# Kernel optimization log

Measured on AMD Instinct MI355X. Metric: run time of the kernel, lower is better.

Reference implementation:

```python
import jax, jax.numpy as jnp
import numpy as np
from jax import lax

K = 5          # kernel_size
P = K // 2     # padding
DN = ('NCHW', 'OIHW', 'NCHW')


def _dwconv(z, wt, bt):
    # depthwise conv: z [b,c,h,w], wt [c,1,K,K], bt [c]
    c = z.shape[1]
    y = lax.conv_general_dilated(z, wt, (1, 1), [(P, P), (P, P)],
                                 feature_group_count=c, dimension_numbers=DN)
    return y + bt[None, :, None, None]


def setup_inputs() -> dict:
    key = jax.random.key(0)
    ks = jax.random.split(key, 8)
    b, c, h, w = 8, 64, 256, 256
    return {
        'x': jax.random.normal(ks[0], (b, c, h, w), jnp.float32),
        'w1': jax.random.normal(ks[1], (3, c, 1, K, K), jnp.float32) * 0.1,
        'b1': jax.random.normal(ks[2], (3, c), jnp.float32) * 0.1,
        'w2': jax.random.normal(ks[3], (3, c, 1, K, K), jnp.float32) * 0.1,
        'b2': jax.random.normal(ks[4], (3, c), jnp.float32) * 0.1,
        'wk': jax.random.normal(ks[5], (K * K * c, c), jnp.float32) * 0.1,
        'bk': jax.random.normal(ks[6], (K * K * c,), jnp.float32) * 0.1,
        'bias': jnp.zeros((c,), jnp.float32),
    }


def reference(x, w1, b1, w2, b2, wk, bk, bias):
    b, c, h, w = x.shape
    # avgpool 2x2 stride 2
    t = x.reshape(b, c, h // 2, 2, w // 2, 2).mean(axis=(3, 5))
    # Block1: 3 depthwise convs
    for i in range(3):
        t = _dwconv(t, w1[i], b1[i])
    # maxpool 2x2 stride 2
    hh, ww = t.shape[2], t.shape[3]
    t = t.reshape(b, c, hh // 2, 2, ww // 2, 2).max(axis=(3, 5))
    # Block2: 3 depthwise convs
    for i in range(3):
        t = _dwconv(t, w2[i], b2[i])
    # adaptive avg pool to 1x1 -> [b, c]
    g = t.mean(axis=(2, 3))
    # tokernel 1x1 conv -> per-sample depthwise kernels [b*c, 1, K, K]
    kern = (jnp.einsum('bc,oc->bo', g, wk) + bk).reshape(b * c, 1, K, K)
    # per-sample dynamic depthwise conv (groups = b*c)
    y = lax.conv_general_dilated(x.reshape(1, b * c, h, w), kern, (1, 1),
                                 [(P, P), (P, P)], feature_group_count=b * c,
                                 dimension_numbers=DN)
    return y.reshape(b, c, h, w) + bias[None, :, None, None]
```

## Files before the change

kernel.cpp:

```cpp
#include <hip/hip_runtime.h>

#define CC 64
#define HH 256
#define WW 256
#define SROW 140
#define BROW 76

template<int SS>
__device__ __forceinline__ void conv4x4_e12(const float* __restrict__ rb,
                                            const float* __restrict__ w,
                                            float bv, float a[4][4])
{
#pragma unroll
    for (int i = 0; i < 4; i++)
#pragma unroll
        for (int j = 0; j < 4; j++) a[i][j] = bv;
#pragma unroll
    for (int ir = 0; ir < 8; ir++) {
        const float* s = rb + ir * SS;
        float4 A = *(const float4*)s;
        float4 B = *(const float4*)(s + 4);
        float4 C = *(const float4*)(s + 8);
        float e[12] = {A.x, A.y, A.z, A.w, B.x, B.y, B.z, B.w,
                       C.x, C.y, C.z, C.w};
#pragma unroll
        for (int i = 0; i < 4; i++) {
            const int ky = ir - i;
            if (ky >= 0 && ky < 5) {
#pragma unroll
                for (int kx = 0; kx < 5; kx++) {
                    const float wv = w[ky * 5 + kx];
#pragma unroll
                    for (int j = 0; j < 4; j++) a[i][j] += e[j + kx + 2] * wv;
                }
            }
        }
    }
}

__device__ __forceinline__ void conv1x4_e12B(const float* __restrict__ rb,
                                             const float* __restrict__ w,
                                             float bv, float a[4])
{
#pragma unroll
    for (int j = 0; j < 4; j++) a[j] = bv;
#pragma unroll
    for (int ir = 0; ir < 5; ir++) {
        const float* s = rb + ir * BROW;
        float4 A = *(const float4*)s;
        float4 B = *(const float4*)(s + 4);
        float4 C = *(const float4*)(s + 8);
        float e[12] = {A.x, A.y, A.z, A.w, B.x, B.y, B.z, B.w,
                       C.x, C.y, C.z, C.w};
#pragma unroll
        for (int kx = 0; kx < 5; kx++) {
            const float wv = w[ir * 5 + kx];
#pragma unroll
            for (int j = 0; j < 4; j++) a[j] += e[j + kx + 2] * wv;
        }
    }
}

__global__ __launch_bounds__(512, 4) void k_keff(
    const float* __restrict__ w2, const float* __restrict__ b2,
    float* __restrict__ kq, float* __restrict__ beta)
{
    const int c = blockIdx.x;
    const int tid = threadIdx.x;
    __shared__ __align__(16) float sb[68 * BROW];
    __shared__ float red[16];

    for (int i = tid; i < 68 * 19; i += 512) {
        int r = i / 19, q = i % 19;
        int d = 4 * q;
        float4 v = make_float4(0.f, 0.f, 0.f, 0.f);
        if (r >= 2 && r < 66 && d >= 8 && d < 72)
            v = make_float4(1.f, 1.f, 1.f, 1.f);
        *(float4*)&sb[r * BROW + d] = v;
    }
    __syncthreads();

    const int r0 = tid >> 4;
    const int u = tid & 15;
    float S0 = 0.f, S1 = 0.f;

#pragma unroll
    for (int step = 0; step < 2; step++) {
        const int cv = 2 - step;
        float w[25];
#pragma unroll
        for (int k = 0; k < 25; k++) w[k] = w2[cv * CC * 25 + c * 25 + (24 - k)];
        float a0[4], a1[4];
        conv1x4_e12B(&sb[r0 * BROW + 4 * u + 4], w, 0.f, a0);
        conv1x4_e12B(&sb[(r0 + 32) * BROW + 4 * u + 4], w, 0.f, a1);
        __syncthreads();
        *(float4*)&sb[(r0 + 2) * BROW + 8 + 4 * u] = make_float4(a0[0], a0[1], a0[2], a0[3]);
        *(float4*)&sb[(r0 + 34) * BROW + 8 + 4 * u] = make_float4(a1[0], a1[1], a1[2], a1[3]);
        float s = a0[0] + a0[1] + a0[2] + a0[3] + a1[0] + a1[1] + a1[2] + a1[3];
        if (step == 0) S0 += s; else S1 += s;
        __syncthreads();
    }

    {
        float w[25];
#pragma unroll
        for (int k = 0; k < 25; k++) w[k] = w2[0 * CC * 25 + c * 25 + (24 - k)];
        float a0[4], a1[4];
        conv1x4_e12B(&sb[r0 * BROW + 4 * u + 4], w, 0.f, a0);
        conv1x4_e12B(&sb[(r0 + 32) * BROW + 4 * u + 4], w, 0.f, a1);
        __syncthreads();
        *(float4*)&sb[(r0 + 2) * BROW + 8 + 4 * u] = make_float4(a0[0], a0[1], a0[2], a0[3]);
        *(float4*)&sb[(r0 + 34) * BROW + 8 + 4 * u] = make_float4(a1[0], a1[1], a1[2], a1[3]);
        __syncthreads();
    }

    for (int i = tid; i < 1024; i += 512) {
        int v = i >> 5, uu = i & 31;
        float k00 = sb[(2 * v + 2) * BROW + 8 + 2 * uu];
        float k01 = sb[(2 * v + 2) * BROW + 8 + 2 * uu + 1];
        float k10 = sb[(2 * v + 3) * BROW + 8 + 2 * uu];
        float k11 = sb[(2 * v + 3) * BROW + 8 + 2 * uu + 1];
        *(float4*)&kq[((size_t)(c * 32 + v) * 32 + uu) * 4] =
            make_float4(k00 * (1.f / 4096.f), k01 * (1.f / 4096.f),
                        k10 * (1.f / 4096.f), k11 * (1.f / 4096.f));
    }

#pragma unroll
    for (int off = 32; off > 0; off >>= 1) {
        S0 += __shfl_down(S0, off);
        S1 += __shfl_down(S1, off);
    }
    if ((tid & 63) == 0) { red[tid >> 6] = S0; red[8 + (tid >> 6)] = S1; }
    __syncthreads();
    if (tid == 0) {
        float t0 = 0.f, t1 = 0.f;
#pragma unroll
        for (int k = 0; k < 8; k++) { t0 += red[k]; t1 += red[8 + k]; }
        beta[c] = (b2[0 * CC + c] * t1 + b2[1 * CC + c] * t0 +
                   4096.f * b2[2 * CC + c]) * (1.f / 4096.f);
    }
}

__global__ __launch_bounds__(1024, 8) void k_a(
    const float* __restrict__ x, const float* __restrict__ w1,
    const float* __restrict__ b1, const float* __restrict__ kq,
    const float* __restrict__ beta, float* __restrict__ g)
{
    const int plane = blockIdx.x;
    const int c = plane & 63;
    const int tid = threadIdx.x;

    __shared__ __align__(16) float sb[132 * SROW];
    __shared__ float red[16];

    const float* xp = x + (size_t)plane * HH * WW;

#pragma unroll
    for (int k = 0; k < 5; k++) {
        int i = tid + k * 1024;
        if (i < 132 * 35) {
            int r = i / 35, f = i % 35;
            int d = 4 * f;
            float4 v = make_float4(0.f, 0.f, 0.f, 0.f);
            int p = r - 2;
            if (d >= 8 && d < 136 && (unsigned)p < 128u) {
                int xc = 2 * (d - 8);
                const float* p0 = xp + (size_t)(2 * p) * WW + xc;
                const float* p1 = p0 + WW;
                float4 a0 = *(const float4*)p0;
                float4 a1 = *(const float4*)(p0 + 4);
                float4 b0 = *(const float4*)p1;
                float4 b1v = *(const float4*)(p1 + 4);
                v.x = 0.25f * (a0.x + a0.y + b0.x + b0.y);
                v.y = 0.25f * (a0.z + a0.w + b0.z + b0.w);
                v.z = 0.25f * (a1.x + a1.y + b1v.x + b1v.y);
                v.w = 0.25f * (a1.z + a1.w + b1v.z + b1v.w);
            }
            *(float4*)&sb[r * SROW + d] = v;
        }
    }
    __syncthreads();

    const int v = tid >> 5, u = tid & 31;
    const float* rbA = &sb[(4 * v) * SROW + 4 * u + 4];
    float* wbA = &sb[(4 * v + 2) * SROW + 8 + 4 * u];

#pragma unroll
    for (int cv = 0; cv < 2; cv++) {
        float w[25];
#pragma unroll
        for (int k = 0; k < 25; k++) w[k] = w1[cv * CC * 25 + c * 25 + k];
        const float bv = b1[cv * CC + c];
        float a[4][4];
        conv4x4_e12<SROW>(rbA, w, bv, a);
        __syncthreads();
#pragma unroll
        for (int i = 0; i < 4; i++)
            *(float4*)(wbA + i * SROW) = make_float4(a[i][0], a[i][1], a[i][2], a[i][3]);
        __syncthreads();
    }

    float partial;
    {
        float w[25];
#pragma unroll
        for (int k = 0; k < 25; k++) w[k] = w1[2 * CC * 25 + c * 25 + k];
        const float bv = b1[2 * CC + c];
        float a[4][4];
        conv4x4_e12<SROW>(rbA, w, bv, a);
        float m00 = fmaxf(fmaxf(a[0][0], a[0][1]), fmaxf(a[1][0], a[1][1]));
        float m01 = fmaxf(fmaxf(a[0][2], a[0][3]), fmaxf(a[1][2], a[1][3]));
        float m10 = fmaxf(fmaxf(a[2][0], a[2][1]), fmaxf(a[3][0], a[3][1]));
        float m11 = fmaxf(fmaxf(a[2][2], a[2][3]), fmaxf(a[3][2], a[3][3]));
        float4 kk = *(const float4*)&kq[((size_t)(c * 32 + v) * 32 + u) * 4];
        partial = m00 * kk.x + m01 * kk.y + m10 * kk.z + m11 * kk.w;
    }
#pragma unroll
    for (int off = 32; off > 0; off >>= 1) partial += __shfl_down(partial, off);
    if ((tid & 63) == 0) red[tid >> 6] = partial;
    __syncthreads();
    if (tid == 0) {
        float t = 0.f;
#pragma unroll
        for (int k = 0; k < 16; k++) t += red[k];
        g[plane] = t + beta[c];
    }
}

__global__ __launch_bounds__(256) void k_kern(
    const float* __restrict__ g, const float* __restrict__ wk,
    const float* __restrict__ bk, float* __restrict__ kern)
{
    const int o = blockIdx.x * 256 + threadIdx.x;
    const int b = o / 1600, oo = o - b * 1600;
    float v = bk[oo];
    const float* wp = wk + (size_t)oo * 64;
    const float* gp = g + b * 64;
#pragma unroll 16
    for (int k = 0; k < 64; k++) v += gp[k] * wp[k];
    kern[o] = v;
}

__global__ __launch_bounds__(256) void k_dyn(
    const float* __restrict__ x, const float* __restrict__ kern,
    const float* __restrict__ bias, float* __restrict__ out)
{
    const int plane = blockIdx.z;
    const int tx = blockIdx.x, ty = blockIdx.y;
    const int tid = threadIdx.x;

    __shared__ __align__(16) float sx[68 * 76];

    const float* xp = x + (size_t)plane * HH * WW;
    const int R0 = ty * 64, C0 = tx * 64;

#pragma unroll
    for (int k = 0; k < 5; k++) {
        int i = tid + k * 256;
        if (i < 68 * 18) {
            int r = i / 18, q = i - r * 18;
            int gr = R0 - 2 + r;
            int gc = C0 - 4 + 4 * q;
            float4 v = make_float4(0.f, 0.f, 0.f, 0.f);
            if ((unsigned)gr < HH && (unsigned)gc < WW)
                v = *(const float4*)(xp + (size_t)gr * WW + gc);
            *(float4*)&sx[r * 76 + 4 * q] = v;
        }
    }

    float w[25];
#pragma unroll
    for (int k = 0; k < 25; k++) w[k] = kern[(size_t)plane * 25 + k];
    const float bv = bias[plane & 63];

    __syncthreads();

    const int tr = (tid >> 4) * 4, tc = (tid & 15) * 4;
    float acc[4][4];
    conv4x4_e12<76>(&sx[tr * 76 + tc], w, bv, acc);

    float* op = out + (size_t)plane * HH * WW + (size_t)(R0 + tr) * WW + C0 + tc;
#pragma unroll
    for (int i = 0; i < 4; i++)
        *(float4*)(op + (size_t)i * WW) = make_float4(acc[i][0], acc[i][1], acc[i][2], acc[i][3]);
}

extern "C" void kernel_launch(void* const* d_in, const int* in_sizes, int n_in,
                              void* d_out, int out_size, void* d_ws, size_t ws_size,
                              hipStream_t stream)
{
    const float* x    = (const float*)d_in[0];
    const float* w1   = (const float*)d_in[1];
    const float* b1   = (const float*)d_in[2];
    const float* w2   = (const float*)d_in[3];
    const float* b2   = (const float*)d_in[4];
    const float* wk   = (const float*)d_in[5];
    const float* bk   = (const float*)d_in[6];
    const float* bias = (const float*)d_in[7];
    float* out = (float*)d_out;

    float* ws   = (float*)d_ws;
    float* kq   = ws;
    float* beta = ws + 262144;
    float* g    = ws + 262208;
    float* kern = ws + 262720;

    k_keff<<<dim3(64), 512, 0, stream>>>(w2, b2, kq, beta);
    k_a<<<dim3(512), 1024, 0, stream>>>(x, w1, b1, kq, beta, g);
    k_kern<<<dim3(50), 256, 0, stream>>>(g, wk, bk, kern);
    k_dyn<<<dim3(4, 4, 512), 256, 0, stream>>>(x, kern, bias, out);
}
```

Measured before the change: 114.6 us.

## Split k_a into half-plane row tiles with halo recompute and 4x8 register tiles

The pooled-branch kernel now processes each plane as two 64-row halves with a 6-row halo, using 512 threads and a smaller shared buffer. The halo rows are recomputed across the three chained convolutions, with the active thread count shrinking at each stage. Each thread now computes a 4x8 output tile instead of 4x4, which improves reuse of the loaded row segments. Partial sums per half are reduced in k_kern, which now runs one block per batch and caches g in shared memory. The intent is better occupancy and latency hiding, at the cost of redundant halo compute and idle threads in the later stages.

```diff
diff --git a/kernel.cpp b/kernel.cpp
--- a/kernel.cpp
+++ b/kernel.cpp
@@ -5,6 +5,29 @@
 #define WW 256
 #define SROW 140
 #define BROW 76
+
+__device__ __forceinline__ void conv1x4_e12B(const float* __restrict__ rb,
+                                             const float* __restrict__ w,
+                                             float bv, float a[4])
+{
+#pragma unroll
+    for (int j = 0; j < 4; j++) a[j] = bv;
+#pragma unroll
+    for (int ir = 0; ir < 5; ir++) {
+        const float* s = rb + ir * BROW;
+        float4 A = *(const float4*)s;
+        float4 B = *(const float4*)(s + 4);
+        float4 C = *(const float4*)(s + 8);
+        float e[12] = {A.x, A.y, A.z, A.w, B.x, B.y, B.z, B.w,
+                       C.x, C.y, C.z, C.w};
+#pragma unroll
+        for (int kx = 0; kx < 5; kx++) {
+            const float wv = w[ir * 5 + kx];
+#pragma unroll
+            for (int j = 0; j < 4; j++) a[j] += e[j + kx + 2] * wv;
+        }
+    }
+}
 
 template<int SS>
 __device__ __forceinline__ void conv4x4_e12(const float* __restrict__ rb,
@@ -38,25 +61,34 @@
     }
 }
 
-__device__ __forceinline__ void conv1x4_e12B(const float* __restrict__ rb,
-                                             const float* __restrict__ w,
-                                             float bv, float a[4])
-{
-#pragma unroll
-    for (int j = 0; j < 4; j++) a[j] = bv;
-#pragma unroll
-    for (int ir = 0; ir < 5; ir++) {
-        const float* s = rb + ir * BROW;
-        float4 A = *(const float4*)s;
-        float4 B = *(const float4*)(s + 4);
-        float4 C = *(const float4*)(s + 8);
-        float e[12] = {A.x, A.y, A.z, A.w, B.x, B.y, B.z, B.w,
-                       C.x, C.y, C.z, C.w};
-#pragma unroll
-        for (int kx = 0; kx < 5; kx++) {
-            const float wv = w[ir * 5 + kx];
-#pragma unroll
-            for (int j = 0; j < 4; j++) a[j] += e[j + kx + 2] * wv;
+__device__ __forceinline__ void conv4x8_e16(const float* __restrict__ rb,
+                                            const float* __restrict__ w,
+                                            float bv, float a[4][8])
+{
+#pragma unroll
+    for (int i = 0; i < 4; i++)
+#pragma unroll
+        for (int j = 0; j < 8; j++) a[i][j] = bv;
+#pragma unroll
+    for (int ir = 0; ir < 8; ir++) {
+        const float* s = rb + ir * SROW;
+        float e[16];
+#pragma unroll
+        for (int m = 0; m < 4; m++) {
+            float4 t = *(const float4*)(s + 4 * m);
+            e[4 * m] = t.x; e[4 * m + 1] = t.y; e[4 * m + 2] = t.z; e[4 * m + 3] = t.w;
+        }
+#pragma unroll
+        for (int i = 0; i < 4; i++) {
+            const int ky = ir - i;
+            if (ky >= 0 && ky < 5) {
+#pragma unroll
+                for (int kx = 0; kx < 5; kx++) {
+                    const float wv = w[ky * 5 + kx];
+#pragma unroll
+                    for (int j = 0; j < 8; j++) a[i][j] += e[j + kx + 2] * wv;
+                }
+            }
         }
     }
 }
@@ -100,7 +132,6 @@
         if (step == 0) S0 += s; else S1 += s;
         __syncthreads();
     }
-
     {
         float w[25];
 #pragma unroll
@@ -141,31 +172,33 @@
     }
 }
 
-__global__ __launch_bounds__(1024, 8) void k_a(
+__global__ __launch_bounds__(512, 6) void k_a(
     const float* __restrict__ x, const float* __restrict__ w1,
     const float* __restrict__ b1, const float* __restrict__ kq,
-    const float* __restrict__ beta, float* __restrict__ g)
-{
-    const int plane = blockIdx.x;
+    float* __restrict__ part)
+{
+    const int by = blockIdx.x;
+    const int plane = blockIdx.y;
     const int c = plane & 63;
+    const int R0 = by * 64;
     const int tid = threadIdx.x;
 
-    __shared__ __align__(16) float sb[132 * SROW];
-    __shared__ float red[16];
+    __shared__ __align__(16) float sb[76 * SROW];
+    __shared__ float red[8];
 
     const float* xp = x + (size_t)plane * HH * WW;
 
 #pragma unroll
-    for (int k = 0; k < 5; k++) {
-        int i = tid + k * 1024;
-        if (i < 132 * 35) {
+    for (int k = 0; k < 6; k++) {
+        int i = tid + k * 512;
+        if (i < 76 * 35) {
             int r = i / 35, f = i % 35;
             int d = 4 * f;
             float4 v = make_float4(0.f, 0.f, 0.f, 0.f);
-            int p = r - 2;
-            if (d >= 8 && d < 136 && (unsigned)p < 128u) {
+            int pr = R0 - 6 + r;
+            if (d >= 8 && d < 136 && (unsigned)pr < 128u) {
                 int xc = 2 * (d - 8);
-                const float* p0 = xp + (size_t)(2 * p) * WW + xc;
+                const float* p0 = xp + (size_t)(2 * pr) * WW + xc;
                 const float* p1 = p0 + WW;
                 float4 a0 = *(const float4*)p0;
                 float4 a1 = *(const float4*)(p0 + 4);
@@ -181,39 +214,89 @@
     }
     __syncthreads();
 
-    const int v = tid >> 5, u = tid & 31;
-    const float* rbA = &sb[(4 * v) * SROW + 4 * u + 4];
-    float* wbA = &sb[(4 * v + 2) * SROW + 8 + 4 * u];
-
-#pragma unroll
-    for (int cv = 0; cv < 2; cv++) {
-        float w[25];
-#pragma unroll
-        for (int k = 0; k < 25; k++) w[k] = w1[cv * CC * 25 + c * 25 + k];
-        const float bv = b1[cv * CC + c];
-        float a[4][4];
-        conv4x4_e12<SROW>(rbA, w, bv, a);
-        __syncthreads();
-#pragma unroll
-        for (int i = 0; i < 4; i++)
-            *(float4*)(wbA + i * SROW) = make_float4(a[i][0], a[i][1], a[i][2], a[i][3]);
-        __syncthreads();
-    }
-
-    float partial;
+    const int v = tid >> 4, u = tid & 15;
+
     {
         float w[25];
 #pragma unroll
+        for (int k = 0; k < 25; k++) w[k] = w1[0 * CC * 25 + c * 25 + k];
+        const float bv = b1[0 * CC + c];
+        const bool act = tid < 288;
+        float a[4][8];
+        if (act) {
+            conv4x8_e16(&sb[(4 * v) * SROW + 4 + 8 * u], w, bv, a);
+#pragma unroll
+            for (int i = 0; i < 4; i++) {
+                int gi = R0 - 4 + 4 * v + i;
+                if ((unsigned)gi >= 128u) {
+#pragma unroll
+                    for (int j = 0; j < 8; j++) a[i][j] = 0.f;
+                }
+            }
+        }
+        __syncthreads();
+        if (act) {
+#pragma unroll
+            for (int i = 0; i < 4; i++) {
+                float* row = &sb[(2 + 4 * v + i) * SROW + 8 + 8 * u];
+                *(float4*)row = make_float4(a[i][0], a[i][1], a[i][2], a[i][3]);
+                *(float4*)(row + 4) = make_float4(a[i][4], a[i][5], a[i][6], a[i][7]);
+            }
+        }
+        __syncthreads();
+    }
+
+    {
+        float w[25];
+#pragma unroll
+        for (int k = 0; k < 25; k++) w[k] = w1[1 * CC * 25 + c * 25 + k];
+        const float bv = b1[1 * CC + c];
+        const bool act = tid < 272;
+        float a[4][8];
+        if (act) {
+            conv4x8_e16(&sb[(2 + 4 * v) * SROW + 4 + 8 * u], w, bv, a);
+#pragma unroll
+            for (int i = 0; i < 4; i++) {
+                int gi = R0 - 2 + 4 * v + i;
+                if ((unsigned)gi >= 128u) {
+#pragma unroll
+                    for (int j = 0; j < 8; j++) a[i][j] = 0.f;
+                }
+            }
+        }
+        __syncthreads();
+        if (act) {
+#pragma unroll
+            for (int i = 0; i < 4; i++) {
+                float* row = &sb[(4 + 4 * v + i) * SROW + 8 + 8 * u];
+                *(float4*)row = make_float4(a[i][0], a[i][1], a[i][2], a[i][3]);
+                *(float4*)(row + 4) = make_float4(a[i][4], a[i][5], a[i][6], a[i][7]);
+            }
+        }
+        __syncthreads();
+    }
+
+    float partial = 0.f;
+    if (tid < 256) {
+        float w[25];
+#pragma unroll
         for (int k = 0; k < 25; k++) w[k] = w1[2 * CC * 25 + c * 25 + k];
         const float bv = b1[2 * CC + c];
-        float a[4][4];
-        conv4x4_e12<SROW>(rbA, w, bv, a);
-        float m00 = fmaxf(fmaxf(a[0][0], a[0][1]), fmaxf(a[1][0], a[1][1]));
-        float m01 = fmaxf(fmaxf(a[0][2], a[0][3]), fmaxf(a[1][2], a[1][3]));
-        float m10 = fmaxf(fmaxf(a[2][0], a[2][1]), fmaxf(a[3][0], a[3][1]));
-        float m11 = fmaxf(fmaxf(a[2][2], a[2][3]), fmaxf(a[3][2], a[3][3]));
-        float4 kk = *(const float4*)&kq[((size_t)(c * 32 + v) * 32 + u) * 4];
-        partial = m00 * kk.x + m01 * kk.y + m10 * kk.z + m11 * kk.w;
+        float a[4][8];
+        conv4x8_e16(&sb[(4 + 4 * v) * SROW + 4 + 8 * u], w, bv, a);
+        float m[2][4];
+#pragma unroll
+        for (int p = 0; p < 2; p++)
+#pragma unroll
+            for (int q = 0; q < 4; q++)
+                m[p][q] = fmaxf(fmaxf(a[2 * p][2 * q], a[2 * p][2 * q + 1]),
+                                fmaxf(a[2 * p + 1][2 * q], a[2 * p + 1][2 * q + 1]));
+        const int V = (R0 >> 2) + v;
+        const int U0 = 2 * u;
+        float4 k0 = *(const float4*)&kq[((size_t)(c * 32 + V) * 32 + U0) * 4];
+        float4 k1 = *(const float4*)&kq[((size_t)(c * 32 + V) * 32 + U0 + 1) * 4];
+        partial = m[0][0] * k0.x + m[0][1] * k0.y + m[1][0] * k0.z + m[1][1] * k0.w
+                + m[0][2] * k1.x + m[0][3] * k1.y + m[1][2] * k1.z + m[1][3] * k1.w;
     }
 #pragma unroll
     for (int off = 32; off > 0; off >>= 1) partial += __shfl_down(partial, off);
@@ -222,23 +305,31 @@
     if (tid == 0) {
         float t = 0.f;
 #pragma unroll
-        for (int k = 0; k < 16; k++) t += red[k];
-        g[plane] = t + beta[c];
+        for (int k = 0; k < 8; k++) t += red[k];
+        part[plane * 2 + by] = t;
     }
 }
 
 __global__ __launch_bounds__(256) void k_kern(
-    const float* __restrict__ g, const float* __restrict__ wk,
-    const float* __restrict__ bk, float* __restrict__ kern)
-{
-    const int o = blockIdx.x * 256 + threadIdx.x;
-    const int b = o / 1600, oo = o - b * 1600;
-    float v = bk[oo];
-    const float* wp = wk + (size_t)oo * 64;
-    const float* gp = g + b * 64;
-#pragma unroll 16
-    for (int k = 0; k < 64; k++) v += gp[k] * wp[k];
-    kern[o] = v;
+    const float* __restrict__ part, const float* __restrict__ beta,
+    const float* __restrict__ wk, const float* __restrict__ bk,
+    float* __restrict__ kern)
+{
+    const int b = blockIdx.x;
+    const int tid = threadIdx.x;
+    __shared__ float sg[64];
+    if (tid < 64) {
+        int plane = b * 64 + tid;
+        sg[tid] = beta[tid] + part[plane * 2] + part[plane * 2 + 1];
+    }
+    __syncthreads();
+    for (int o = tid; o < 1600; o += 256) {
+        float v = bk[o];
+        const float* wp = wk + (size_t)o * 64;
+#pragma unroll 8
+        for (int k = 0; k < 64; k++) v += sg[k] * wp[k];
+        kern[b * 1600 + o] = v;
+    }
 }
 
 __global__ __launch_bounds__(256) void k_dyn(
@@ -302,11 +393,11 @@
     float* ws   = (float*)d_ws;
     float* kq   = ws;
     float* beta = ws + 262144;
-    float* g    = ws + 262208;
-    float* kern = ws + 262720;
+    float* part = ws + 262208;
+    float* kern = ws + 263232;
 
     k_keff<<<dim3(64), 512, 0, stream>>>(w2, b2, kq, beta);
-    k_a<<<dim3(512), 1024, 0, stream>>>(x, w1, b1, kq, beta, g);
-    k_kern<<<dim3(50), 256, 0, stream>>>(g, wk, bk, kern);
+    k_a<<<dim3(2, 512), 512, 0, stream>>>(x, w1, b1, kq, part);
+    k_kern<<<dim3(8), 256, 0, stream>>>(part, beta, wk, bk, kern);
     k_dyn<<<dim3(4, 4, 512), 256, 0, stream>>>(x, kern, bias, out);
 }
```

Result: slower. 259.0 us (+126.0%).
